# Kernel optimization log

Measured on AMD Instinct MI355X. Metric: run time of the kernel, lower is better.

Reference implementation:

```python
import jax, jax.numpy as jnp
import numpy as np
from jax import lax

STRIDE = (1, 1)
PADDING = ((1, 1), (1, 1))
DILATION = (1, 1)


def setup_inputs() -> dict:
    key = jax.random.key(0)
    k1, k2 = jax.random.split(key)
    input = jax.random.normal(k1, (32, 128, 56, 56), dtype=jnp.float32)
    weight = jax.random.normal(k2, (256, 128, 3, 3), dtype=jnp.float32)
    bias = jnp.zeros((256,), dtype=jnp.float32)
    return {"input": input, "weight": weight, "bias": bias}


def reference(input, weight, bias):
    # The original builds the conv's dense matrix via conv2d on an identity
    # basis and then matmuls; that is mathematically identical to a direct
    # conv2d (the map is linear), plus the broadcast bias.
    out = lax.conv_general_dilated(
        input, weight,
        window_strides=STRIDE,
        padding=PADDING,
        rhs_dilation=DILATION,
        dimension_numbers=("NCHW", "OIHW", "NCHW"),
    )
    return out + bias[None, :, None, None]
```

## Files before the change

kernel.cpp:

```cpp
#include <hip/hip_runtime.h>
#include <hip/hip_bf16.h>
#include <stdint.h>


typedef __attribute__((ext_vector_type(8))) short bf16x8;
typedef __attribute__((ext_vector_type(8))) unsigned short ushort8;
typedef __attribute__((ext_vector_type(4))) float f32x4;

#define HW       56
#define SPATIAL  3136
#define C_IN     128
#define K_OUT    256
#define GEMM_K   1152
#define GEMM_N   100352

#define PHW      58
#define PIMG     3364
#define PADTOT_AL 107656

#define BM       256
#define BN       128
#define NTILE    18
#define BUFH     24576

__device__ __forceinline__ unsigned short f2bf(float f) {
    union { float f; unsigned int u; } v; v.f = f;
    unsigned int u = v.u + 0x7FFFu + ((v.u >> 16) & 1u);
    return (unsigned short)(u >> 16);
}

__device__ __forceinline__ void gload16(const unsigned short* g, unsigned short* l) {
    __builtin_amdgcn_global_load_lds(
        (const __attribute__((address_space(1))) unsigned int*)(g),
        (__attribute__((address_space(3))) unsigned int*)(l),
        16, 0, 0);
}

__global__ void wtrans_kernel(const float* __restrict__ w, unsigned short* __restrict__ w3) {
    int idx = blockIdx.x * 256 + threadIdx.x;
    int rc   = idx / 18432;
    int rem  = idx % 18432;
    int tap  = rem / 2048;
    int rem2 = rem % 2048;
    int cc   = rem2 / 512;
    int s    = rem2 % 512;
    int l    = s >> 3, j = s & 7;
    int ko   = rc * 16 + (l & 15);
    int c    = cc * 32 + ((l >> 4) << 3) + j;
    w3[idx] = f2bf(w[(ko * C_IN + c) * 9 + tap]);
}

__global__ __launch_bounds__(256)
void border_zero(unsigned short* __restrict__ pad) {
    int idx = blockIdx.x * 256 + threadIdx.x;
    if (idx >= 29184) return;
    int cc  = idx / 7296;
    int r   = idx % 7296;
    int img = r / 228;
    int p   = r % 228;
    int pos;
    if (p < 58)       pos = p;
    else if (p < 116) pos = 57 * PHW + (p - 58);
    else { int i = p - 116; pos = (1 + (i >> 1)) * PHW + (i & 1) * 57; }
    unsigned short* d = pad + (size_t)cc * PADTOT_AL * 32
                      + ((size_t)img * PIMG + pos) * 32;
    const ushort8 z = (ushort8){0,0,0,0,0,0,0,0};
    *reinterpret_cast<ushort8*>(d)      = z;
    *reinterpret_cast<ushort8*>(d + 8)  = z;
    *reinterpret_cast<ushort8*>(d + 16) = z;
    *reinterpret_cast<ushort8*>(d + 24) = z;
}

__global__ __launch_bounds__(256)
void intrans_kernel(const float* __restrict__ in, unsigned short* __restrict__ pad) {
    __shared__ __attribute__((aligned(16))) unsigned short l[56 * 136];
    const int bx = blockIdx.x;
    const int n = bx / HW, h = bx % HW;
    const int tid = threadIdx.x;
    const float* src = in + (size_t)n * C_IN * SPATIAL + h * HW;
    #pragma unroll
    for (int i = 0; i < 28; ++i) {
        int idx = i * 256 + tid;
        int c = idx / HW, w = idx % HW;
        l[w * 136 + c] = f2bf(src[(size_t)c * SPATIAL + w]);
    }
    __syncthreads();
    const int prow = n * PIMG + (h + 1) * PHW;
    #pragma unroll
    for (int j = 0; j < 4; ++j) {
        int chunk = j * 256 + tid;
        if (chunk < 896) {
            int w = chunk >> 4, c8 = chunk & 15;
            int cc = c8 >> 2, sub = c8 & 3;
            unsigned short* dst = pad + (size_t)cc * PADTOT_AL * 32
                                + (size_t)(prow + w + 1) * 32 + sub * 8;
            *reinterpret_cast<ushort8*>(dst) =
                *reinterpret_cast<const ushort8*>(&l[w * 136 + c8 * 8]);
        }
    }
}

__global__ __launch_bounds__(512, 2)
void conv_m201(const unsigned short* __restrict__ pad,
               const unsigned short* __restrict__ w3,
               const float* __restrict__ bias,
               float* __restrict__ out) {
    __shared__ __attribute__((aligned(16))) unsigned short lds[2 * BUFH];

    const int tid  = threadIdx.x;
    const int wave = tid >> 6;
    const int lane = tid & 63;
    const int la   = lane & 15;
    const int lkh  = lane >> 4;

    const int bid = blockIdx.x;
    const int nt  = (bid & 7) * 98 + (bid >> 3);
    const int g0  = nt * BN;

    const int wr = wave >> 1, wc = wave & 1;

    const unsigned short* aw0 = w3 + (size_t)(wave * 2 + 0) * 18432 + lane * 8;
    const unsigned short* aw1 = w3 + (size_t)(wave * 2 + 1) * 18432 + lane * 8;
    const unsigned short* bsrc;
    {
        int col = g0 + wave * 16 + la;
        int img = col / SPATIAL;
        int pos = col - img * SPATIAL;
        int oh  = pos / HW, ow = pos - oh * HW;
        bsrc = pad + (size_t)(img * PIMG + (oh + 1) * PHW + (ow + 1)) * 32 + lkh * 8;
    }

    f32x4 acc[4][4];
    #pragma unroll
    for (int i = 0; i < 4; ++i)
        #pragma unroll
        for (int j = 0; j < 4; ++j)
            acc[i][j] = (f32x4){0.f, 0.f, 0.f, 0.f};

    auto STAGE = [&](int tn, int kc) {
        const int tap = tn >> 1;
        const int cc  = (tn & 1) * 2 + kc;
        const int dr = tap / 3 - 1, dsx = tap % 3 - 1;
        unsigned short* dst = &lds[(tn & 1) * BUFH];
        gload16(aw0 + (size_t)(tap * 4 + cc) * 512, dst + (wave * 4 + kc) * 512);
        gload16(aw1 + (size_t)(tap * 4 + cc) * 512, dst + (wave * 4 + 2 + kc) * 512);
        gload16(bsrc + (size_t)cc * PADTOT_AL * 32 + (dr * PHW + dsx) * 32,
                dst + 16384 + (wave * 2 + kc) * 512);
    };

    STAGE(0, 0); STAGE(0, 1);
    asm volatile("s_waitcnt vmcnt(0)" ::: "memory");
    __builtin_amdgcn_s_barrier();

    #pragma unroll
    for (int t = 0; t < NTILE; ++t) {
        const unsigned short* Ab = &lds[(t & 1) * BUFH];
        #pragma unroll
        for (int ks = 0; ks < 2; ++ks) {
            bf16x8 af[4], bv[4];
            #pragma unroll
            for (int mi = 0; mi < 4; ++mi)
                af[mi] = *reinterpret_cast<const bf16x8*>(
                    &Ab[((wr * 4 + mi) * 2 + ks) * 512 + lane * 8]);
            #pragma unroll
            for (int nj = 0; nj < 4; ++nj)
                bv[nj] = *reinterpret_cast<const bf16x8*>(
                    &Ab[16384 + ((wc * 4 + nj) * 2 + ks) * 512 + lane * 8]);

            if (t + 1 < NTILE) STAGE(t + 1, ks);

            __builtin_amdgcn_s_barrier();
            asm volatile("s_waitcnt lgkmcnt(0)" ::: "memory");
            __builtin_amdgcn_sched_barrier(0);

            __builtin_amdgcn_s_setprio(1);
            #pragma unroll
            for (int mi = 0; mi < 4; ++mi)
                #pragma unroll
                for (int nj = 0; nj < 4; ++nj)
                    acc[mi][nj] = __builtin_amdgcn_mfma_f32_16x16x32_bf16(
                        af[mi], bv[nj], acc[mi][nj], 0, 0, 0);
            __builtin_amdgcn_s_setprio(0);

            if (ks == 1 && t + 1 < NTILE)
                asm volatile("s_waitcnt vmcnt(0)" ::: "memory");
            __builtin_amdgcn_s_barrier();
        }
    }

    #pragma unroll
    for (int mi = 0; mi < 4; ++mi) {
        const int mb = wr * 64 + mi * 16 + lkh * 4;
        const f32x4 bv4 = *reinterpret_cast<const f32x4*>(&bias[mb]);
        #pragma unroll
        for (int nj = 0; nj < 4; ++nj) {
            const int gcol = g0 + wc * 64 + nj * 16;
            const int n2 = gcol / SPATIAL;
            const int p2 = gcol - n2 * SPATIAL + la;
            float* op = out + ((size_t)(n2 * K_OUT + mb)) * SPATIAL + p2;
            op[0]                   = acc[mi][nj][0] + bv4[0];
            op[SPATIAL]             = acc[mi][nj][1] + bv4[1];
            op[2 * SPATIAL]         = acc[mi][nj][2] + bv4[2];
            op[3 * (size_t)SPATIAL] = acc[mi][nj][3] + bv4[3];
        }
    }
}

#define LDK 40
__global__ __launch_bounds__(256)
void conv_mfma_fallback(const float* __restrict__ in,
                        const float* __restrict__ wraw,
                        const float* __restrict__ bias,
                        float* __restrict__ out) {
    __shared__ __attribute__((aligned(16))) unsigned short lA[128 * LDK];
    __shared__ __attribute__((aligned(16))) unsigned short lB[128 * LDK];
    const int tid = threadIdx.x;
    const int m0  = blockIdx.y * 128;
    const int g0  = blockIdx.x * 128;
    const int wave = tid >> 6, lane = tid & 63;
    const int wr = wave >> 1, wc = wave & 1;
    const int la = lane & 15, lkh = lane >> 4, lk = lkh * 8;

    f32x4 acc[4][4];
    #pragma unroll
    for (int i = 0; i < 4; ++i)
        #pragma unroll
        for (int j = 0; j < 4; ++j)
            acc[i][j] = (f32x4){0.f, 0.f, 0.f, 0.f};

    const int jj = tid & 127;
    const int kb = (tid >> 7) * 16;
    const int g = g0 + jj;
    const int nimg = g / SPATIAL;
    const int pos  = g % SPATIAL;
    const int oh = pos / HW, ow = pos % HW;

    for (int tap = 0; tap < 9; ++tap) {
        const int dr = tap / 3 - 1, dsx = tap % 3 - 1;
        const int ih = oh + dr, iw = ow + dsx;
        const bool valid = ((unsigned)ih < HW) && ((unsigned)iw < HW);
        const float* src = in + ((nimg * C_IN) * HW + ih) * HW + iw;
        for (int c0 = 0; c0 < C_IN; c0 += 32) {
            #pragma unroll
            for (int i = 0; i < 2; ++i) {
                const int ch = tid * 2 + i;
                const int row = ch >> 2;
                const int kp = (ch & 3) * 8;
                ushort8 v;
                #pragma unroll
                for (int e = 0; e < 8; ++e)
                    v[e] = f2bf(wraw[((m0 + row) * C_IN + c0 + kp + e) * 9 + tap]);
                *reinterpret_cast<ushort8*>(&lA[row * LDK + kp]) = v;
            }
            {
                ushort8 v0, v1;
                #pragma unroll
                for (int i = 0; i < 8; ++i)
                    v0[i] = f2bf(valid ? src[(c0 + kb + i) * SPATIAL] : 0.f);
                #pragma unroll
                for (int i = 0; i < 8; ++i)
                    v1[i] = f2bf(valid ? src[(c0 + kb + 8 + i) * SPATIAL] : 0.f);
                *reinterpret_cast<ushort8*>(&lB[jj * LDK + kb])     = v0;
                *reinterpret_cast<ushort8*>(&lB[jj * LDK + kb + 8]) = v1;
            }
            __syncthreads();
            bf16x8 af[4], bv[4];
            #pragma unroll
            for (int f = 0; f < 4; ++f) {
                af[f] = *reinterpret_cast<const bf16x8*>(&lA[(wr * 64 + f * 16 + la) * LDK + lk]);
                bv[f] = *reinterpret_cast<const bf16x8*>(&lB[(wc * 64 + f * 16 + la) * LDK + lk]);
            }
            #pragma unroll
            for (int fi = 0; fi < 4; ++fi)
                #pragma unroll
                for (int fj = 0; fj < 4; ++fj)
                    acc[fi][fj] = __builtin_amdgcn_mfma_f32_16x16x32_bf16(
                        af[fi], bv[fj], acc[fi][fj], 0, 0, 0);
            __syncthreads();
        }
    }
    const int mbase = m0 + wr * 64;
    const int cbase = g0 + wc * 64;
    #pragma unroll
    for (int fi = 0; fi < 4; ++fi) {
        float bvv[4];
        #pragma unroll
        for (int r = 0; r < 4; ++r)
            bvv[r] = bias[mbase + fi * 16 + lkh * 4 + r];
        #pragma unroll
        for (int fj = 0; fj < 4; ++fj) {
            const int gcol = cbase + fj * 16 + la;
            const int n2 = gcol / SPATIAL;
            const int p2 = gcol % SPATIAL;
            float* op = out + (size_t)(n2 * K_OUT) * SPATIAL + p2;
            #pragma unroll
            for (int r = 0; r < 4; ++r)
                op[(size_t)(mbase + fi * 16 + lkh * 4 + r) * SPATIAL] = acc[fi][fj][r] + bvv[r];
        }
    }
}

extern "C" void kernel_launch(void* const* d_in, const int* in_sizes, int n_in,
                              void* d_out, int out_size, void* d_ws, size_t ws_size,
                              hipStream_t stream) {
    const float* in   = (const float*)d_in[0];
    const float* w    = (const float*)d_in[1];
    const float* bias = (const float*)d_in[2];
    float* out = (float*)d_out;

    const size_t pad_halves = 4ull * PADTOT_AL * 32ull;
    const size_t need_bytes = (pad_halves + 294912ull) * 2ull;

    if (ws_size >= need_bytes) {
        unsigned short* pad = (unsigned short*)d_ws;
        unsigned short* w3  = pad + pad_halves;
        border_zero<<<114, 256, 0, stream>>>(pad);
        wtrans_kernel<<<294912 / 256, 256, 0, stream>>>(w, w3);
        intrans_kernel<<<32 * HW, 256, 0, stream>>>(in, pad);
        conv_m201<<<GEMM_N / BN, 512, 0, stream>>>(pad, w3, bias, out);
    } else {
        dim3 grid(GEMM_N / 128, K_OUT / 128);
        conv_mfma_fallback<<<grid, 256, 0, stream>>>(in, w, bias, out);
    }
}
```

Before: 113.7 us.

## Widen conv GEMM tile to 256x256 and prefetch half-stages two tiles ahead

Doubles the N tile so each block computes a 256x256 output tile with a 2x4 wave layout and 8x4 MFMA accumulators per wave. This raises operand reuse per LDS byte and halves the number of blocks. The loop is also restructured: each iteration loads both K-halves' A fragments up front, and the next tile's second half plus the tile after next's first half are issued mid-iteration, with partial vmcnt/lgkmcnt waits. In exchange, LDS use per block grows to 128 KB and register pressure rises sharply. The grid of 392 blocks also balances less evenly across CUs.

Result: faster. 98.21 us (-13.6%).

```diff
diff --git a/kernel.cpp b/kernel.cpp
--- a/kernel.cpp
+++ b/kernel.cpp
@@ -19,9 +19,9 @@
 #define PADTOT_AL 107656
 
 #define BM       256
-#define BN       128
+#define BN       256
 #define NTILE    18
-#define BUFH     24576
+#define BUFH     32768
 
 __device__ __forceinline__ unsigned short f2bf(float f) {
     union { float f; unsigned int u; } v; v.f = f;
@@ -101,7 +101,7 @@
 }
 
 __global__ __launch_bounds__(512, 2)
-void conv_m201(const unsigned short* __restrict__ pad,
+void conv_m256(const unsigned short* __restrict__ pad,
                const unsigned short* __restrict__ w3,
                const float* __restrict__ bias,
                float* __restrict__ out) {
@@ -114,25 +114,31 @@
     const int lkh  = lane >> 4;
 
     const int bid = blockIdx.x;
-    const int nt  = (bid & 7) * 98 + (bid >> 3);
+    const int nt  = (bid & 7) * 49 + (bid >> 3);
     const int g0  = nt * BN;
 
-    const int wr = wave >> 1, wc = wave & 1;
+    const int wr = wave >> 2, wc = wave & 3;
 
     const unsigned short* aw0 = w3 + (size_t)(wave * 2 + 0) * 18432 + lane * 8;
     const unsigned short* aw1 = w3 + (size_t)(wave * 2 + 1) * 18432 + lane * 8;
-    const unsigned short* bsrc;
+    const unsigned short* bsrc0;
+    const unsigned short* bsrc1;
     {
-        int col = g0 + wave * 16 + la;
+        int col = g0 + (wave * 2 + 0) * 16 + la;
         int img = col / SPATIAL;
         int pos = col - img * SPATIAL;
         int oh  = pos / HW, ow = pos - oh * HW;
-        bsrc = pad + (size_t)(img * PIMG + (oh + 1) * PHW + (ow + 1)) * 32 + lkh * 8;
-    }
-
-    f32x4 acc[4][4];
-    #pragma unroll
-    for (int i = 0; i < 4; ++i)
+        bsrc0 = pad + (size_t)(img * PIMG + (oh + 1) * PHW + (ow + 1)) * 32 + lkh * 8;
+        col = g0 + (wave * 2 + 1) * 16 + la;
+        img = col / SPATIAL;
+        pos = col - img * SPATIAL;
+        oh  = pos / HW; ow = pos - oh * HW;
+        bsrc1 = pad + (size_t)(img * PIMG + (oh + 1) * PHW + (ow + 1)) * 32 + lkh * 8;
+    }
+
+    f32x4 acc[8][4];
+    #pragma unroll
+    for (int i = 0; i < 8; ++i)
         #pragma unroll
         for (int j = 0; j < 4; ++j)
             acc[i][j] = (f32x4){0.f, 0.f, 0.f, 0.f};
@@ -142,55 +148,79 @@
         const int cc  = (tn & 1) * 2 + kc;
         const int dr = tap / 3 - 1, dsx = tap % 3 - 1;
         unsigned short* dst = &lds[(tn & 1) * BUFH];
-        gload16(aw0 + (size_t)(tap * 4 + cc) * 512, dst + (wave * 4 + kc) * 512);
-        gload16(aw1 + (size_t)(tap * 4 + cc) * 512, dst + (wave * 4 + 2 + kc) * 512);
-        gload16(bsrc + (size_t)cc * PADTOT_AL * 32 + (dr * PHW + dsx) * 32,
-                dst + 16384 + (wave * 2 + kc) * 512);
+        const ptrdiff_t bofs = (ptrdiff_t)cc * PADTOT_AL * 32 + (dr * PHW + dsx) * 32;
+        gload16(aw0 + (size_t)(tap * 4 + cc) * 512, dst + ((wave * 2 + 0) * 2 + kc) * 512);
+        gload16(aw1 + (size_t)(tap * 4 + cc) * 512, dst + ((wave * 2 + 1) * 2 + kc) * 512);
+        gload16(bsrc0 + bofs, dst + 16384 + ((wave * 2 + 0) * 2 + kc) * 512);
+        gload16(bsrc1 + bofs, dst + 16384 + ((wave * 2 + 1) * 2 + kc) * 512);
     };
 
-    STAGE(0, 0); STAGE(0, 1);
-    asm volatile("s_waitcnt vmcnt(0)" ::: "memory");
+    bf16x8 af0[8], af1[8], bv0[4], bv1[4];
+
+    STAGE(0, 0); STAGE(0, 1); STAGE(1, 0);
+    asm volatile("s_waitcnt vmcnt(4)" ::: "memory");
     __builtin_amdgcn_s_barrier();
 
     #pragma unroll
     for (int t = 0; t < NTILE; ++t) {
         const unsigned short* Ab = &lds[(t & 1) * BUFH];
-        #pragma unroll
-        for (int ks = 0; ks < 2; ++ks) {
-            bf16x8 af[4], bv[4];
-            #pragma unroll
-            for (int mi = 0; mi < 4; ++mi)
-                af[mi] = *reinterpret_cast<const bf16x8*>(
-                    &Ab[((wr * 4 + mi) * 2 + ks) * 512 + lane * 8]);
+
+        #pragma unroll
+        for (int mi = 0; mi < 8; ++mi)
+            af0[mi] = *reinterpret_cast<const bf16x8*>(
+                &Ab[((wr * 8 + mi) * 2 + 0) * 512 + lane * 8]);
+        #pragma unroll
+        for (int nj = 0; nj < 4; ++nj)
+            bv0[nj] = *reinterpret_cast<const bf16x8*>(
+                &Ab[16384 + ((wc * 4 + nj) * 2 + 0) * 512 + lane * 8]);
+        #pragma unroll
+        for (int mi = 0; mi < 8; ++mi)
+            af1[mi] = *reinterpret_cast<const bf16x8*>(
+                &Ab[((wr * 8 + mi) * 2 + 1) * 512 + lane * 8]);
+
+        asm volatile("s_waitcnt lgkmcnt(8)" ::: "memory");
+        __builtin_amdgcn_sched_barrier(0);
+        __builtin_amdgcn_s_setprio(1);
+        #pragma unroll
+        for (int mi = 0; mi < 8; ++mi)
             #pragma unroll
             for (int nj = 0; nj < 4; ++nj)
-                bv[nj] = *reinterpret_cast<const bf16x8*>(
-                    &Ab[16384 + ((wc * 4 + nj) * 2 + ks) * 512 + lane * 8]);
-
-            if (t + 1 < NTILE) STAGE(t + 1, ks);
-
+                acc[mi][nj] = __builtin_amdgcn_mfma_f32_16x16x32_bf16(
+                    af0[mi], bv0[nj], acc[mi][nj], 0, 0, 0);
+        __builtin_amdgcn_s_setprio(0);
+
+        __builtin_amdgcn_s_barrier();
+
+        #pragma unroll
+        for (int nj = 0; nj < 4; ++nj)
+            bv1[nj] = *reinterpret_cast<const bf16x8*>(
+                &Ab[16384 + ((wc * 4 + nj) * 2 + 1) * 512 + lane * 8]);
+        if (t + 1 < NTILE) STAGE(t + 1, 1);
+        if (t + 2 < NTILE) STAGE(t + 2, 0);
+
+        asm volatile("s_waitcnt lgkmcnt(0)" ::: "memory");
+        __builtin_amdgcn_sched_barrier(0);
+        __builtin_amdgcn_s_setprio(1);
+        #pragma unroll
+        for (int mi = 0; mi < 8; ++mi)
+            #pragma unroll
+            for (int nj = 0; nj < 4; ++nj)
+                acc[mi][nj] = __builtin_amdgcn_mfma_f32_16x16x32_bf16(
+                    af1[mi], bv1[nj], acc[mi][nj], 0, 0, 0);
+        __builtin_amdgcn_s_setprio(0);
+
+        if (t < NTILE - 2) {
+            asm volatile("s_waitcnt vmcnt(4)" ::: "memory");
             __builtin_amdgcn_s_barrier();
-            asm volatile("s_waitcnt lgkmcnt(0)" ::: "memory");
-            __builtin_amdgcn_sched_barrier(0);
-
-            __builtin_amdgcn_s_setprio(1);
-            #pragma unroll
-            for (int mi = 0; mi < 4; ++mi)
-                #pragma unroll
-                for (int nj = 0; nj < 4; ++nj)
-                    acc[mi][nj] = __builtin_amdgcn_mfma_f32_16x16x32_bf16(
-                        af[mi], bv[nj], acc[mi][nj], 0, 0, 0);
-            __builtin_amdgcn_s_setprio(0);
-
-            if (ks == 1 && t + 1 < NTILE)
-                asm volatile("s_waitcnt vmcnt(0)" ::: "memory");
+        } else if (t == NTILE - 2) {
+            asm volatile("s_waitcnt vmcnt(0)" ::: "memory");
             __builtin_amdgcn_s_barrier();
         }
     }
 
     #pragma unroll
-    for (int mi = 0; mi < 4; ++mi) {
-        const int mb = wr * 64 + mi * 16 + lkh * 4;
+    for (int mi = 0; mi < 8; ++mi) {
+        const int mb = wr * 128 + mi * 16 + lkh * 4;
         const f32x4 bv4 = *reinterpret_cast<const f32x4*>(&bias[mb]);
         #pragma unroll
         for (int nj = 0; nj < 4; ++nj) {
@@ -317,7 +347,7 @@
         border_zero<<<114, 256, 0, stream>>>(pad);
         wtrans_kernel<<<294912 / 256, 256, 0, stream>>>(w, w3);
         intrans_kernel<<<32 * HW, 256, 0, stream>>>(in, pad);
-        conv_m201<<<GEMM_N / BN, 512, 0, stream>>>(pad, w3, bias, out);
+        conv_m256<<<GEMM_N / BN, 512, 0, stream>>>(pad, w3, bias, out);
     } else {
         dim3 grid(GEMM_N / 128, K_OUT / 128);
         conv_mfma_fallback<<<grid, 256, 0, stream>>>(in, w, bias, out);
```

## Replace LDS-staged conv GEMM with direct global-to-register fragment loads

Applied to the files above, without the earlier changes.

Drops LDS double buffering and barriers in the implicit-GEMM conv. Each wave now loads its MFMA A and B fragments straight from global memory into registers. The output tile goes from 256x128 with 512 threads to 128x128 with 256 threads, so the grid doubles and the block swizzle is adjusted. This removes synchronisation overhead, but every wave now fetches its own operands, so global and L2 traffic go up and there is no explicit prefetch to hide load latency.

After: 134.6 us. 1.18x slower.

```diff
diff --git a/kernel.cpp b/kernel.cpp
--- a/kernel.cpp
+++ b/kernel.cpp
@@ -18,22 +18,12 @@
 #define PIMG     3364
 #define PADTOT_AL 107656
 
-#define BM       256
-#define BN       128
 #define NTILE    18
-#define BUFH     24576
 
 __device__ __forceinline__ unsigned short f2bf(float f) {
     union { float f; unsigned int u; } v; v.f = f;
     unsigned int u = v.u + 0x7FFFu + ((v.u >> 16) & 1u);
     return (unsigned short)(u >> 16);
-}
-
-__device__ __forceinline__ void gload16(const unsigned short* g, unsigned short* l) {
-    __builtin_amdgcn_global_load_lds(
-        (const __attribute__((address_space(1))) unsigned int*)(g),
-        (__attribute__((address_space(3))) unsigned int*)(l),
-        16, 0, 0);
 }
 
 __global__ void wtrans_kernel(const float* __restrict__ w, unsigned short* __restrict__ w3) {
@@ -100,13 +90,11 @@
     }
 }
 
-__global__ __launch_bounds__(512, 2)
-void conv_m201(const unsigned short* __restrict__ pad,
-               const unsigned short* __restrict__ w3,
-               const float* __restrict__ bias,
-               float* __restrict__ out) {
-    __shared__ __attribute__((aligned(16))) unsigned short lds[2 * BUFH];
-
+__global__ __launch_bounds__(256, 3)
+void conv_direct(const unsigned short* __restrict__ pad,
+                 const unsigned short* __restrict__ w3,
+                 const float* __restrict__ bias,
+                 float* __restrict__ out) {
     const int tid  = threadIdx.x;
     const int wave = tid >> 6;
     const int lane = tid & 63;
@@ -114,20 +102,26 @@
     const int lkh  = lane >> 4;
 
     const int bid = blockIdx.x;
-    const int nt  = (bid & 7) * 98 + (bid >> 3);
-    const int g0  = nt * BN;
+    const int swz = (bid & 7) * 196 + (bid >> 3);
+    const int mt  = swz & 1, nt = swz >> 1;
+    const int m0  = mt * 128;
+    const int g0  = nt * 128;
 
     const int wr = wave >> 1, wc = wave & 1;
 
-    const unsigned short* aw0 = w3 + (size_t)(wave * 2 + 0) * 18432 + lane * 8;
-    const unsigned short* aw1 = w3 + (size_t)(wave * 2 + 1) * 18432 + lane * 8;
-    const unsigned short* bsrc;
-    {
-        int col = g0 + wave * 16 + la;
+    const unsigned short* asrc[4];
+    #pragma unroll
+    for (int mi = 0; mi < 4; ++mi)
+        asrc[mi] = w3 + (size_t)((m0 >> 4) + wr * 4 + mi) * 18432 + lane * 8;
+
+    const unsigned short* bsrc[4];
+    #pragma unroll
+    for (int bc = 0; bc < 4; ++bc) {
+        int col = g0 + wc * 64 + bc * 16 + la;
         int img = col / SPATIAL;
         int pos = col - img * SPATIAL;
         int oh  = pos / HW, ow = pos - oh * HW;
-        bsrc = pad + (size_t)(img * PIMG + (oh + 1) * PHW + (ow + 1)) * 32 + lkh * 8;
+        bsrc[bc] = pad + (size_t)(img * PIMG + (oh + 1) * PHW + (ow + 1)) * 32 + lkh * 8;
     }
 
     f32x4 acc[4][4];
@@ -137,60 +131,39 @@
         for (int j = 0; j < 4; ++j)
             acc[i][j] = (f32x4){0.f, 0.f, 0.f, 0.f};
 
-    auto STAGE = [&](int tn, int kc) {
-        const int tap = tn >> 1;
-        const int cc  = (tn & 1) * 2 + kc;
+    #pragma unroll
+    for (int t = 0; t < NTILE; ++t) {
+        const int tap = t >> 1;
         const int dr = tap / 3 - 1, dsx = tap % 3 - 1;
-        unsigned short* dst = &lds[(tn & 1) * BUFH];
-        gload16(aw0 + (size_t)(tap * 4 + cc) * 512, dst + (wave * 4 + kc) * 512);
-        gload16(aw1 + (size_t)(tap * 4 + cc) * 512, dst + (wave * 4 + 2 + kc) * 512);
-        gload16(bsrc + (size_t)cc * PADTOT_AL * 32 + (dr * PHW + dsx) * 32,
-                dst + 16384 + (wave * 2 + kc) * 512);
-    };
-
-    STAGE(0, 0); STAGE(0, 1);
-    asm volatile("s_waitcnt vmcnt(0)" ::: "memory");
-    __builtin_amdgcn_s_barrier();
-
-    #pragma unroll
-    for (int t = 0; t < NTILE; ++t) {
-        const unsigned short* Ab = &lds[(t & 1) * BUFH];
+        bf16x8 a[4][2], b[4][2];
         #pragma unroll
         for (int ks = 0; ks < 2; ++ks) {
-            bf16x8 af[4], bv[4];
+            const int cc = (t & 1) * 2 + ks;
+            const ptrdiff_t aofs = (ptrdiff_t)(tap * 4 + cc) * 512;
+            const ptrdiff_t bofs = (ptrdiff_t)cc * (PADTOT_AL * 32)
+                                 + (dr * PHW + dsx) * 32;
             #pragma unroll
             for (int mi = 0; mi < 4; ++mi)
-                af[mi] = *reinterpret_cast<const bf16x8*>(
-                    &Ab[((wr * 4 + mi) * 2 + ks) * 512 + lane * 8]);
-            #pragma unroll
-            for (int nj = 0; nj < 4; ++nj)
-                bv[nj] = *reinterpret_cast<const bf16x8*>(
-                    &Ab[16384 + ((wc * 4 + nj) * 2 + ks) * 512 + lane * 8]);
-
-            if (t + 1 < NTILE) STAGE(t + 1, ks);
-
-            __builtin_amdgcn_s_barrier();
-            asm volatile("s_waitcnt lgkmcnt(0)" ::: "memory");
-            __builtin_amdgcn_sched_barrier(0);
-
-            __builtin_amdgcn_s_setprio(1);
+                a[mi][ks] = *reinterpret_cast<const bf16x8*>(asrc[mi] + aofs);
+            #pragma unroll
+            for (int bc = 0; bc < 4; ++bc)
+                b[bc][ks] = *reinterpret_cast<const bf16x8*>(bsrc[bc] + bofs);
+        }
+        __builtin_amdgcn_s_setprio(1);
+        #pragma unroll
+        for (int ks = 0; ks < 2; ++ks)
             #pragma unroll
             for (int mi = 0; mi < 4; ++mi)
                 #pragma unroll
                 for (int nj = 0; nj < 4; ++nj)
                     acc[mi][nj] = __builtin_amdgcn_mfma_f32_16x16x32_bf16(
-                        af[mi], bv[nj], acc[mi][nj], 0, 0, 0);
-            __builtin_amdgcn_s_setprio(0);
-
-            if (ks == 1 && t + 1 < NTILE)
-                asm volatile("s_waitcnt vmcnt(0)" ::: "memory");
-            __builtin_amdgcn_s_barrier();
-        }
+                        a[mi][ks], b[nj][ks], acc[mi][nj], 0, 0, 0);
+        __builtin_amdgcn_s_setprio(0);
     }
 
     #pragma unroll
     for (int mi = 0; mi < 4; ++mi) {
-        const int mb = wr * 64 + mi * 16 + lkh * 4;
+        const int mb = m0 + wr * 64 + mi * 16 + lkh * 4;
         const f32x4 bv4 = *reinterpret_cast<const f32x4*>(&bias[mb]);
         #pragma unroll
         for (int nj = 0; nj < 4; ++nj) {
@@ -317,7 +290,7 @@
         border_zero<<<114, 256, 0, stream>>>(pad);
         wtrans_kernel<<<294912 / 256, 256, 0, stream>>>(w, w3);
         intrans_kernel<<<32 * HW, 256, 0, stream>>>(in, pad);
-        conv_m201<<<GEMM_N / BN, 512, 0, stream>>>(pad, w3, bias, out);
+        conv_direct<<<(GEMM_N / 128) * (K_OUT / 128), 256, 0, stream>>>(pad, w3, bias, out);
     } else {
         dim3 grid(GEMM_N / 128, K_OUT / 128);
         conv_mfma_fallback<<<grid, 256, 0, stream>>>(in, w, bias, out);
```
